# Performance work log

Hardware: AMD Instinct MI355X
Metric: run time of the kernel (lower is better)

## Reference

```python
import jax, jax.numpy as jnp
import numpy as np

B, T, D = 2, 2048, 1024
H, HD = 16, 32
INNER = H * HD
FF = 4 * D
KT, KP = 3, 15


def _layernorm(x, g, b, eps=1e-5):
    mu = jnp.mean(x, axis=-1, keepdims=True)
    var = jnp.var(x, axis=-1, keepdims=True)
    return (x - mu) * jax.lax.rsqrt(var + eps) * g + b


def _causal_dwconv(x, w, b):
    # x: (b,t,d), w: (d,1,k) depthwise kernel; causal left-pad of k-1
    k = w.shape[-1]
    xc = jnp.transpose(x, (0, 2, 1))  # (b,d,t)
    xp = jnp.pad(xc, ((0, 0), (0, 0), (k - 1, 0)))
    y = jax.lax.conv_general_dilated(
        xp, w, window_strides=(1,), padding='VALID',
        feature_group_count=x.shape[-1],
        dimension_numbers=('NCH', 'OIH', 'NCH'))
    return jnp.transpose(y + b[None, :, None], (0, 2, 1))


def _causal_linear_attention(q, k, v, mask):
    # q,k,v: (b,t,h,d); mask: (b,t)
    m = mask[:, :, None, None]
    q = (jax.nn.elu(q) + 1.0) * m
    k = (jax.nn.elu(k) + 1.0) * m
    v = v * m
    kv = jnp.einsum('bthd,bthe->bthde', k, v)
    kv_prefix = jnp.cumsum(kv, axis=1)          # (b,t,h,d,e) large intermediate
    k_prefix = jnp.cumsum(k, axis=1)
    num = jnp.einsum('bthd,bthde->bthe', q, kv_prefix)
    den = jnp.sum(q * k_prefix, axis=-1, keepdims=True)
    return (num / (den + 1e-6)) * m


def setup_inputs() -> dict:
    key = jax.random.key(0)
    ks = jax.random.split(key, 10)
    w = lambda i, shape: jax.random.normal(ks[i], shape, jnp.float32) * 0.02
    return {
        'inputs': jax.random.normal(ks[0], (B, T, D), jnp.float32),
        'mask': jnp.ones((B, T), jnp.float32),
        'ln1_g': jnp.ones((D,), jnp.float32), 'ln1_b': jnp.zeros((D,), jnp.float32),
        'W_in': w(1, (D, D + 3 * INNER)), 'b_in': jnp.zeros((D + 3 * INNER,), jnp.float32),
        'W_c': w(2, (INNER, D)), 'b_c': jnp.zeros((D,), jnp.float32),
        'w_t': w(3, (D, 1, KT)), 'b_t': jnp.zeros((D,), jnp.float32),
        'w_p': w(4, (D, 1, KP)), 'b_p': jnp.zeros((D,), jnp.float32),
        'W_mix': w(5, (3 * D, D)), 'b_mix': jnp.zeros((D,), jnp.float32),
        'ln2_g': jnp.ones((D,), jnp.float32), 'ln2_b': jnp.zeros((D,), jnp.float32),
        'W1': w(6, (D, FF)), 'b1': jnp.zeros((FF,), jnp.float32),
        'W2': w(7, (FF, D)), 'b2': jnp.zeros((D,), jnp.float32),
    }


def reference(inputs, mask, ln1_g, ln1_b, W_in, b_in, W_c, b_c, w_t, b_t,
              w_p, b_p, W_mix, b_mix, ln2_g, ln2_b, W1, b1, W2, b2):
    residual = inputs
    normed = _layernorm(inputs, ln1_g, ln1_b)
    proj = normed @ W_in + b_in
    gate, q, k, v = jnp.split(proj, [D, D + INNER, D + 2 * INNER], axis=-1)
    b, t, _ = inputs.shape
    q = q.reshape(b, t, H, HD)
    k = k.reshape(b, t, H, HD)
    v = v.reshape(b, t, H, HD)
    content = _causal_linear_attention(q, k, v, mask).reshape(b, t, INNER)
    content = content @ W_c + b_c
    temporal = _causal_dwconv(normed, w_t, b_t)
    positional = _causal_dwconv(normed, w_p, b_p)
    mixed = jnp.concatenate((content, temporal, positional), axis=-1) @ W_mix + b_mix
    mask_f = mask[:, :, None]
    out = residual + jax.nn.sigmoid(gate) * mixed  # dropout=0.0 -> identity
    out = out * mask_f
    h = _layernorm(out, ln2_g, ln2_b)
    ffn = jax.nn.gelu(h @ W1 + b1, approximate=False) @ W2 + b2
    out = out + ffn
    return out * mask_f
```

## Files before the change

kernel.cpp:

```cpp
#include <hip/hip_runtime.h>
#include <math.h>

#define BB 2
#define TT 2048
#define DD 1024
#define HH 16
#define INNERD 512
#define FFD 4096
#define NPROJ 2560
#define CATD 3072
#define MROWS (BB*TT)
#define CHUNK 64
#define NCH (TT/CHUNK)
#define BH 32

typedef __bf16 bf16;
typedef __attribute__((ext_vector_type(8))) __bf16 bf16x8;
typedef __attribute__((ext_vector_type(4))) __bf16 bf16x4;
typedef __attribute__((ext_vector_type(4))) float f32x4;

struct Part4 { void* p0; void* p1; void* p2; void* p3; };

__global__ __launch_bounds__(256) void prep_fused(
    const float* __restrict__ inputs, const float* __restrict__ ln1_g,
    const float* __restrict__ ln1_b, bf16* __restrict__ normed,
    const float* __restrict__ W_in,  bf16* __restrict__ wt_in,
    const float* __restrict__ W_c,   bf16* __restrict__ wt_c,
    const float* __restrict__ W_mix, bf16* __restrict__ wt_mix,
    const float* __restrict__ W1,    bf16* __restrict__ wt1,
    const float* __restrict__ W2,    bf16* __restrict__ wt2)
{
    int blk = blockIdx.x, tid = threadIdx.x;
    if (blk < MROWS) {
        int row = blk;
        f32x4 xv = ((const f32x4*)(inputs + (size_t)row * DD))[tid];
        float s = xv[0] + xv[1] + xv[2] + xv[3];
        float s2 = xv[0]*xv[0] + xv[1]*xv[1] + xv[2]*xv[2] + xv[3]*xv[3];
        #pragma unroll
        for (int off = 32; off > 0; off >>= 1) {
            s  += __shfl_xor(s,  off, 64);
            s2 += __shfl_xor(s2, off, 64);
        }
        __shared__ float rs[4], rs2[4];
        int wid = tid >> 6;
        if ((tid & 63) == 0) { rs[wid] = s; rs2[wid] = s2; }
        __syncthreads();
        s  = rs[0] + rs[1] + rs[2] + rs[3];
        s2 = rs2[0] + rs2[1] + rs2[2] + rs2[3];
        float mean = s * (1.0f / DD);
        float var  = s2 * (1.0f / DD) - mean * mean;
        float rstd = rsqrtf(var + 1e-5f);
        f32x4 gv = ((const f32x4*)ln1_g)[tid];
        f32x4 bv = ((const f32x4*)ln1_b)[tid];
        bf16x4 o;
        #pragma unroll
        for (int q = 0; q < 4; q++)
            o[q] = (bf16)((xv[q] - mean) * rstd * gv[q] + bv[q]);
        ((bf16x4*)(normed + (size_t)row * DD))[tid] = o;
        return;
    }
    int tb = blk - MROWS;
    const float* W; bf16* Wt; int Kd, Nd;
    if      (tb < 2560)  {             W = W_in;  Wt = wt_in;  Kd = 1024; Nd = 2560; }
    else if (tb < 3072)  { tb -= 2560; W = W_c;   Wt = wt_c;   Kd = 512;  Nd = 1024; }
    else if (tb < 6144)  { tb -= 3072; W = W_mix; Wt = wt_mix; Kd = 3072; Nd = 1024; }
    else if (tb < 10240) { tb -= 6144; W = W1;    Wt = wt1;    Kd = 1024; Nd = 4096; }
    else                 { tb -= 10240;W = W2;    Wt = wt2;    Kd = 4096; Nd = 1024; }
    int ntx = Nd >> 5;
    int nb = (tb % ntx) * 32, kb = (tb / ntx) * 32;
    __shared__ float t[32][33];
    int tx = tid & 31, ty = tid >> 5;
    #pragma unroll
    for (int r = 0; r < 32; r += 8)
        t[ty + r][tx] = W[(size_t)(kb + ty + r) * Nd + nb + tx];
    __syncthreads();
    #pragma unroll
    for (int r = 0; r < 32; r += 8)
        Wt[(size_t)(nb + ty + r) * Kd + kb + tx] = (bf16)t[tx][ty + r];
}

template<int EPI>
__global__ __launch_bounds__(256, 4) void gemm_mfma(
    const bf16* __restrict__ A,  int lda,
    const bf16* __restrict__ Bt, int ldb,
    const float* __restrict__ bias,
    bf16* __restrict__ Cb, int ldc,
    int K, Part4 part)
{
    __shared__ bf16 As[128 * 64];
    __shared__ bf16 Bs[128 * 64];
    const int tid  = threadIdx.x;
    const int wave = tid >> 6, lane = tid & 63;
    const int m0 = blockIdx.x * 128, n0 = blockIdx.y * 128;
    const int koff = blockIdx.z * K;
    A  += koff;
    Bt += koff;
    const int wr = wave >> 1, wc = wave & 1;
    const int lrow = lane >> 2;
    const int lcol = (lane & 3) * 8;
    const int fm = lane & 15;
    const int fk = (lane >> 4) * 8;

    f32x4 acc[4][4];
    #pragma unroll
    for (int i = 0; i < 4; i++)
        #pragma unroll
        for (int j = 0; j < 4; j++)
            acc[i][j] = (f32x4){0.f, 0.f, 0.f, 0.f};

    for (int k0 = 0; k0 < K; k0 += 64) {
        #pragma unroll
        for (int r = 0; r < 4; r++) {
            int c  = r * 4 + wave;
            int rc = c >> 1, kh = c & 1;
            const bf16* ga = A  + (size_t)(m0 + rc * 16 + lrow) * lda + k0 + kh * 32 + lcol;
            const bf16* gb = Bt + (size_t)(n0 + rc * 16 + lrow) * ldb + k0 + kh * 32 + lcol;
            __builtin_amdgcn_global_load_lds(
                (const __attribute__((address_space(1))) void*)ga,
                (__attribute__((address_space(3))) void*)(As + c * 512), 16, 0, 0);
            __builtin_amdgcn_global_load_lds(
                (const __attribute__((address_space(1))) void*)gb,
                (__attribute__((address_space(3))) void*)(Bs + c * 512), 16, 0, 0);
        }
        __syncthreads();
        #pragma unroll
        for (int ks = 0; ks < 2; ks++) {
            bf16x8 af[4], bfv[4];
            #pragma unroll
            for (int i = 0; i < 4; i++)
                af[i] = *(const bf16x8*)(As + (wr * 4 + i) * 1024 + ks * 512 + fm * 32 + fk);
            #pragma unroll
            for (int j = 0; j < 4; j++)
                bfv[j] = *(const bf16x8*)(Bs + (wc * 4 + j) * 1024 + ks * 512 + fm * 32 + fk);
            #pragma unroll
            for (int i = 0; i < 4; i++)
                #pragma unroll
                for (int j = 0; j < 4; j++)
                    acc[i][j] = __builtin_amdgcn_mfma_f32_16x16x32_bf16(
                        af[i], bfv[j], acc[i][j], 0, 0, 0);
        }
        __syncthreads();
    }

    void* psel = nullptr;
    if constexpr (EPI == 4) {
        int z = blockIdx.z;
        psel = (z == 0) ? part.p0 : (z == 1) ? part.p1 : (z == 2) ? part.p2 : part.p3;
    }

    #pragma unroll
    for (int i = 0; i < 4; i++) {
        int mbase = m0 + wr * 64 + i * 16 + (lane >> 4) * 4;
        #pragma unroll
        for (int j = 0; j < 4; j++) {
            int col = n0 + wc * 64 + j * 16 + (lane & 15);
            float bv = 0.f;
            if constexpr (EPI == 0 || EPI == 1) bv = bias[col];
            #pragma unroll
            for (int r = 0; r < 4; r++) {
                int row = mbase + r;
                float v = acc[i][j][r] + bv;
                if constexpr (EPI == 0) {
                    Cb[(size_t)row * ldc + col] = (bf16)v;
                } else if constexpr (EPI == 1) {
                    float z2 = v * (1.5957691f + 0.07135502f * v * v);
                    v = v / (1.0f + __expf(-z2));
                    Cb[(size_t)row * ldc + col] = (bf16)v;
                } else {
                    ((bf16*)psel)[(size_t)row * DD + col] = (bf16)v;
                }
            }
        }
    }
}

__global__ __launch_bounds__(256) void epi_wc(
    const bf16* __restrict__ P0, const bf16* __restrict__ P1,
    const float* __restrict__ bias, bf16* __restrict__ cat)
{
    int id = blockIdx.x * 256 + threadIdx.x;
    int row = id >> 8, cg = id & 255;
    bf16x4 s0 = ((const bf16x4*)P0)[id];
    bf16x4 s1 = ((const bf16x4*)P1)[id];
    f32x4 b  = ((const f32x4*)bias)[cg];
    bf16x4 o;
    #pragma unroll
    for (int q = 0; q < 4; q++) o[q] = (bf16)((float)s0[q] + (float)s1[q] + b[q]);
    *(bf16x4*)(cat + (size_t)row * CATD + cg * 4) = o;
}

__global__ __launch_bounds__(256) void epi_mix_ln2(
    const bf16* __restrict__ P0, const bf16* __restrict__ P1,
    const bf16* __restrict__ P2, const float* __restrict__ bias,
    const bf16* __restrict__ proj, const float* __restrict__ res,
    const float* __restrict__ mask,
    const float* __restrict__ g2, const float* __restrict__ b2v,
    float* __restrict__ out1, bf16* __restrict__ hbuf)
{
    int row = blockIdx.x, tid = threadIdx.x;
    float m = mask[row];
    size_t off = (size_t)row * DD + tid * 4;
    bf16x4 s0 = *(const bf16x4*)(P0 + off);
    bf16x4 s1 = *(const bf16x4*)(P1 + off);
    bf16x4 s2v = *(const bf16x4*)(P2 + off);
    f32x4 bv = ((const f32x4*)bias)[tid];
    bf16x4 g4 = *(const bf16x4*)(proj + (size_t)row * NPROJ + tid * 4);
    f32x4 rv = ((const f32x4*)(res + (size_t)row * DD))[tid];
    f32x4 v;
    #pragma unroll
    for (int q = 0; q < 4; q++) {
        float sg = 1.0f / (1.0f + __expf(-(float)g4[q]));
        float sv = (float)s0[q] + (float)s1[q] + (float)s2v[q] + bv[q];
        v[q] = (rv[q] + sg * sv) * m;
    }
    ((f32x4*)(out1 + (size_t)row * DD))[tid] = v;
    float s = v[0] + v[1] + v[2] + v[3];
    float s2 = v[0]*v[0] + v[1]*v[1] + v[2]*v[2] + v[3]*v[3];
    #pragma unroll
    for (int off2 = 32; off2 > 0; off2 >>= 1) {
        s  += __shfl_xor(s,  off2, 64);
        s2 += __shfl_xor(s2, off2, 64);
    }
    __shared__ float rs[4], rs2[4];
    int wid = tid >> 6;
    if ((tid & 63) == 0) { rs[wid] = s; rs2[wid] = s2; }
    __syncthreads();
    s  = rs[0] + rs[1] + rs[2] + rs[3];
    s2 = rs2[0] + rs2[1] + rs2[2] + rs2[3];
    float mean = s * (1.0f / DD);
    float var  = s2 * (1.0f / DD) - mean * mean;
    float rstd = rsqrtf(var + 1e-5f);
    f32x4 gg = ((const f32x4*)g2)[tid];
    f32x4 bb = ((const f32x4*)b2v)[tid];
    bf16x4 h;
    #pragma unroll
    for (int q = 0; q < 4; q++)
        h[q] = (bf16)((v[q] - mean) * rstd * gg[q] + bb[q]);
    ((bf16x4*)(hbuf + (size_t)row * DD))[tid] = h;
}

__global__ __launch_bounds__(256) void epi_w2(
    float* __restrict__ d_out, const float* __restrict__ out1,
    const bf16* __restrict__ P0, const bf16* __restrict__ P1,
    const bf16* __restrict__ P2, const bf16* __restrict__ P3,
    const float* __restrict__ bias, const float* __restrict__ mask)
{
    int id = blockIdx.x * 256 + threadIdx.x;
    int row = id >> 8;
    float m = mask[row];
    bf16x4 a0 = ((const bf16x4*)P0)[id];
    bf16x4 a1 = ((const bf16x4*)P1)[id];
    bf16x4 a2 = ((const bf16x4*)P2)[id];
    bf16x4 a3 = ((const bf16x4*)P3)[id];
    f32x4 r = ((const f32x4*)out1)[id];
    f32x4 b = ((const f32x4*)bias)[id & 255];
    f32x4 o;
    #pragma unroll
    for (int q = 0; q < 4; q++) {
        float sv = (float)a0[q] + (float)a1[q] + (float)a2[q] + (float)a3[q];
        o[q] = (r[q] + sv + b[q]) * m;
    }
    ((f32x4*)d_out)[id] = o;
}

__device__ __forceinline__ float phi_f(float x) {
    return x > 0.f ? x + 1.f : __expf(x);
}

__global__ __launch_bounds__(256) void mid_fused(
    const bf16* __restrict__ x,
    const float* __restrict__ w_t, const float* __restrict__ b_t,
    const float* __restrict__ w_p, const float* __restrict__ b_p,
    bf16* __restrict__ cat,
    const bf16* __restrict__ proj, const float* __restrict__ mask,
    float* __restrict__ kvsum, float* __restrict__ kssum)
{
    __shared__ float s_ks[2][CHUNK][32], s_vs[2][CHUNK][32];
    int blk = blockIdx.x, tid = threadIdx.x;
    if (blk < 1024) {
        int id = blk * 256 + tid;
        int cg = id & 127, rp = id >> 7;
        int c0 = cg * 8;
        int row0 = rp * 2;
        int t0 = row0 & (TT - 1);
        bf16x8 xw[16];
        #pragma unroll
        for (int j = 0; j < 16; j++) {
            int t = t0 - 14 + j;
            if (t >= 0)
                xw[j] = *(const bf16x8*)(x + (size_t)(row0 - 14 + j) * DD + c0);
            else
                #pragma unroll
                for (int q = 0; q < 8; q++) xw[j][q] = (bf16)0.f;
        }
        float y15[2][8], y3[2][8];
        #pragma unroll
        for (int q = 0; q < 8; q++) {
            float bp = b_p[c0 + q], bt = b_t[c0 + q];
            y15[0][q] = bp; y15[1][q] = bp;
            y3[0][q] = bt;  y3[1][q] = bt;
        }
        #pragma unroll
        for (int i = 0; i < 15; i++) {
            float wp[8];
            #pragma unroll
            for (int q = 0; q < 8; q++) wp[q] = w_p[(c0 + q) * 15 + i];
            #pragma unroll
            for (int rr = 0; rr < 2; rr++)
                #pragma unroll
                for (int q = 0; q < 8; q++)
                    y15[rr][q] = fmaf(wp[q], (float)xw[rr + i][q], y15[rr][q]);
        }
        #pragma unroll
        for (int i = 0; i < 3; i++) {
            float wt[8];
            #pragma unroll
            for (int q = 0; q < 8; q++) wt[q] = w_t[(c0 + q) * 3 + i];
            #pragma unroll
            for (int rr = 0; rr < 2; rr++)
                #pragma unroll
                for (int q = 0; q < 8; q++)
                    y3[rr][q] = fmaf(wt[q], (float)xw[rr + 12 + i][q], y3[rr][q]);
        }
        #pragma unroll
        for (int rr = 0; rr < 2; rr++) {
            bf16x8 o3, o15;
            #pragma unroll
            for (int q = 0; q < 8; q++) { o3[q] = (bf16)y3[rr][q]; o15[q] = (bf16)y15[rr][q]; }
            *(bf16x8*)(cat + (size_t)(row0 + rr) * CATD + DD + c0)     = o3;
            *(bf16x8*)(cat + (size_t)(row0 + rr) * CATD + 2 * DD + c0) = o15;
        }
        return;
    }
    int w = tid >> 6;
    if (w >= 2) return;
    int lane = tid & 63;
    int ci = (blk - 1024) * 2 + w;
    int c  = ci & (NCH - 1);
    int bh = ci >> 5;
    int b  = bh >> 4, hh = bh & (HH - 1);
    float (*ks)[32] = s_ks[w];
    float (*vs)[32] = s_vs[w];
    int row0 = b * TT + c * CHUNK;
    {
        int row = row0 + lane;
        float m = mask[row];
        const bf16* kp = proj + (size_t)row * NPROJ + DD + INNERD + hh * 32;
        const bf16* vp = kp + INNERD;
        #pragma unroll
        for (int s = 0; s < 4; s++) {
            bf16x8 k8 = *(const bf16x8*)(kp + s * 8);
            bf16x8 v8 = *(const bf16x8*)(vp + s * 8);
            #pragma unroll
            for (int q = 0; q < 8; q++) {
                ks[lane][s * 8 + q] = phi_f((float)k8[q]) * m;
                vs[lane][s * 8 + q] = (float)v8[q] * m;
            }
        }
    }
    int e = lane & 31, d0 = (lane >> 5) * 16;
    float kv[16], ksl[16];
    #pragma unroll
    for (int j = 0; j < 16; j++) { kv[j] = 0.f; ksl[j] = 0.f; }
    for (int t = 0; t < CHUNK; t++) {
        float ve = vs[t][e];
        f32x4 kr[4];
        #pragma unroll
        for (int s = 0; s < 4; s++) kr[s] = *(const f32x4*)&ks[t][d0 + s * 4];
        #pragma unroll
        for (int j = 0; j < 16; j++) {
            float kval = kr[j >> 2][j & 3];
            kv[j] = fmaf(kval, ve, kv[j]);
            ksl[j] += kval;
        }
    }
    size_t base = (size_t)ci * 1024;
    #pragma unroll
    for (int j = 0; j < 16; j++)
        kvsum[base + (size_t)(d0 + j) * 32 + e] = kv[j];
    if (e == 0) {
        #pragma unroll
        for (int j = 0; j < 16; j++)
            kssum[ci * 32 + d0 + j] = ksl[j];
    }
}

__global__ __launch_bounds__(256) void attn_prefix(
    const float* __restrict__ kvsum, const float* __restrict__ kssum,
    float* __restrict__ kvpref, float* __restrict__ kspref)
{
    int bh = blockIdx.x;
    int tid = threadIdx.x;
    float run[4] = {0.f, 0.f, 0.f, 0.f};
    for (int c = 0; c < NCH; c++) {
        size_t base = (size_t)(bh * NCH + c) * 1024 + tid * 4;
        #pragma unroll
        for (int q = 0; q < 4; q++) {
            kvpref[base + q] = run[q];
            run[q] += kvsum[base + q];
        }
    }
    if (tid < 32) {
        float r = 0.f;
        for (int c = 0; c < NCH; c++) {
            kspref[(bh * NCH + c) * 32 + tid] = r;
            r += kssum[(bh * NCH + c) * 32 + tid];
        }
    }
}

__global__ __launch_bounds__(64) void attn_scan(
    const bf16* __restrict__ proj, const float* __restrict__ mask,
    const float* __restrict__ kvpref, const float* __restrict__ kspref,
    bf16* __restrict__ attn_out)
{
    int blk = blockIdx.x;
    int c  = blk & (NCH - 1);
    int bh = blk >> 5;
    int b  = bh >> 4, hh = bh & (HH - 1);
    int lane = threadIdx.x;
    __shared__ float qs[CHUNK][32], ks[CHUNK][32], vs[CHUNK][32];
    __shared__ float ms[CHUNK];
    int row0 = b * TT + c * CHUNK;
    {
        int row = row0 + lane;
        float m = mask[row];
        ms[lane] = m;
        const bf16* qp = proj + (size_t)row * NPROJ + DD + hh * 32;
        const bf16* kp = qp + INNERD;
        const bf16* vp = kp + INNERD;
        #pragma unroll
        for (int s = 0; s < 4; s++) {
            bf16x8 q8 = *(const bf16x8*)(qp + s * 8);
            bf16x8 k8 = *(const bf16x8*)(kp + s * 8);
            bf16x8 v8 = *(const bf16x8*)(vp + s * 8);
            #pragma unroll
            for (int q = 0; q < 8; q++) {
                qs[lane][s * 8 + q] = phi_f((float)q8[q]) * m;
                ks[lane][s * 8 + q] = phi_f((float)k8[q]) * m;
                vs[lane][s * 8 + q] = (float)v8[q] * m;
            }
        }
    }
    int e = lane & 31, d0 = (lane >> 5) * 16;
    float kv[16], ksl[16];
    size_t base = (size_t)blk * 1024;
    #pragma unroll
    for (int j = 0; j < 16; j++) kv[j] = kvpref[base + (size_t)(d0 + j) * 32 + e];
    #pragma unroll
    for (int j = 0; j < 16; j++) ksl[j] = kspref[blk * 32 + d0 + j];
    __syncthreads();
    for (int t = 0; t < CHUNK; t++) {
        float ve = vs[t][e];
        f32x4 kr[4], qr[4];
        #pragma unroll
        for (int s = 0; s < 4; s++) kr[s] = *(const f32x4*)&ks[t][d0 + s * 4];
        #pragma unroll
        for (int s = 0; s < 4; s++) qr[s] = *(const f32x4*)&qs[t][d0 + s * 4];
        float num0 = 0.f, num1 = 0.f, den0 = 0.f, den1 = 0.f;
        #pragma unroll
        for (int j = 0; j < 16; j++) {
            float kval = kr[j >> 2][j & 3], qval = qr[j >> 2][j & 3];
            kv[j]  = fmaf(kval, ve, kv[j]);
            ksl[j] += kval;
            if (j & 1) { num1 = fmaf(qval, kv[j], num1); den1 = fmaf(qval, ksl[j], den1); }
            else       { num0 = fmaf(qval, kv[j], num0); den0 = fmaf(qval, ksl[j], den0); }
        }
        float num = num0 + num1, den = den0 + den1;
        num += __shfl_xor(num, 32, 64);
        den += __shfl_xor(den, 32, 64);
        if (lane < 32)
            attn_out[(size_t)(row0 + t) * INNERD + hh * 32 + e] =
                (bf16)(num / (den + 1e-6f) * ms[t]);
    }
}

extern "C" void kernel_launch(void* const* d_in, const int* in_sizes, int n_in,
                              void* d_out, int out_size, void* d_ws, size_t ws_size,
                              hipStream_t stream)
{
    const float* inputs = (const float*)d_in[0];
    const float* mask   = (const float*)d_in[1];
    const float* ln1_g  = (const float*)d_in[2];
    const float* ln1_b  = (const float*)d_in[3];
    const float* W_in   = (const float*)d_in[4];
    const float* b_in   = (const float*)d_in[5];
    const float* W_c    = (const float*)d_in[6];
    const float* b_c    = (const float*)d_in[7];
    const float* w_t    = (const float*)d_in[8];
    const float* b_t    = (const float*)d_in[9];
    const float* w_p    = (const float*)d_in[10];
    const float* b_p    = (const float*)d_in[11];
    const float* W_mix  = (const float*)d_in[12];
    const float* b_mix  = (const float*)d_in[13];
    const float* ln2_g  = (const float*)d_in[14];
    const float* ln2_b  = (const float*)d_in[15];
    const float* W1     = (const float*)d_in[16];
    const float* b1     = (const float*)d_in[17];
    const float* W2     = (const float*)d_in[18];
    const float* b2     = (const float*)d_in[19];
    float* out = (float*)d_out;

    char* p = (char*)d_ws;
    bf16* normed = (bf16*)p;  p += (size_t)MROWS * DD * 2;
    bf16* proj   = (bf16*)p;  p += (size_t)MROWS * NPROJ * 2;
    bf16* attnb  = (bf16*)p;  p += (size_t)MROWS * INNERD * 2;
    bf16* cat    = (bf16*)p;  p += (size_t)MROWS * CATD * 2;
    float* out1  = (float*)p; p += (size_t)MROWS * DD * 4;
    bf16* hbuf   = (bf16*)p;  p += (size_t)MROWS * DD * 2;
    bf16* wt_in  = (bf16*)p;  p += (size_t)NPROJ * DD * 2;
    bf16* wt_c   = (bf16*)p;  p += (size_t)DD * INNERD * 2;
    bf16* wt_mix = (bf16*)p;  p += (size_t)DD * CATD * 2;
    bf16* wt1    = (bf16*)p;  p += (size_t)FFD * DD * 2;
    bf16* wt2    = (bf16*)p;  p += (size_t)DD * FFD * 2;
    bf16* ffn1   = (bf16*)d_ws;
    float* kvsum = out1;
    float* kvpref= kvsum  + (size_t)BH * NCH * 1024;
    float* kssum = kvpref + (size_t)BH * NCH * 1024;
    float* kspref= kssum  + (size_t)BH * NCH * 32;
    bf16*  c_p0  = (bf16*)d_out;
    bf16*  c_p1  = (bf16*)out1;
    bf16*  m_p0  = (bf16*)d_out;
    bf16*  m_p1  = (bf16*)d_out + (size_t)MROWS * DD;
    bf16*  m_p2  = hbuf;
    bf16*  w2_p0 = cat;
    bf16*  w2_p1 = cat + (size_t)MROWS * DD;
    bf16*  w2_p2 = cat + (size_t)MROWS * DD * 2;
    bf16*  w2_p3 = hbuf;

    prep_fused<<<MROWS + 14336, 256, 0, stream>>>(
        inputs, ln1_g, ln1_b, normed,
        W_in, wt_in, W_c, wt_c, W_mix, wt_mix, W1, wt1, W2, wt2);
    gemm_mfma<0><<<dim3(MROWS/128, NPROJ/128), 256, 0, stream>>>(
        normed, DD, wt_in, DD, b_in, proj, NPROJ, DD, Part4{});
    mid_fused<<<1024 + 512, 256, 0, stream>>>(
        normed, w_t, b_t, w_p, b_p, cat, proj, mask, kvsum, kssum);
    attn_prefix<<<BH, 256, 0, stream>>>(kvsum, kssum, kvpref, kspref);
    attn_scan  <<<BH * NCH, 64, 0, stream>>>(proj, mask, kvpref, kspref, attnb);
    gemm_mfma<4><<<dim3(MROWS/128, DD/128, 2), 256, 0, stream>>>(
        attnb, INNERD, wt_c, INNERD, nullptr, nullptr, DD, INNERD / 2,
        Part4{c_p0, c_p1, nullptr, nullptr});
    epi_wc<<<MROWS * DD / 4 / 256, 256, 0, stream>>>(c_p0, c_p1, b_c, cat);
    gemm_mfma<4><<<dim3(MROWS/128, DD/128, 3), 256, 0, stream>>>(
        cat, CATD, wt_mix, CATD, nullptr, nullptr, DD, CATD / 3,
        Part4{m_p0, m_p1, m_p2, nullptr});
    epi_mix_ln2<<<MROWS, 256, 0, stream>>>(m_p0, m_p1, m_p2, b_mix, proj, inputs,
                                           mask, ln2_g, ln2_b, out1, hbuf);
    gemm_mfma<1><<<dim3(MROWS/128, FFD/128), 256, 0, stream>>>(
        hbuf, DD, wt1, DD, b1, ffn1, FFD, DD, Part4{});
    gemm_mfma<4><<<dim3(MROWS/128, DD/128, 4), 256, 0, stream>>>(
        ffn1, FFD, wt2, FFD, nullptr, nullptr, DD, FFD / 4,
        Part4{w2_p0, w2_p1, w2_p2, w2_p3});
    epi_w2<<<MROWS * DD / 4 / 256, 256, 0, stream>>>(out, out1, w2_p0, w2_p1,
                                                     w2_p2, w2_p3, b2, mask);
}
```

Baseline: 397.0 us.

## Replace GEMM with 256x256 double-buffered swizzled-LDS MFMA kernel

```diff
diff --git a/kernel.cpp b/kernel.cpp
--- a/kernel.cpp
+++ b/kernel.cpp
@@ -79,67 +79,118 @@
         Wt[(size_t)(nb + ty + r) * Kd + kb + tx] = (bf16)t[tx][ty + r];
 }
 
+__device__ __forceinline__ void stage_half(
+    const bf16* __restrict__ src, int ld, int k0, int h_row0,
+    bf16* lds_half, int wave, int rl, int ce)
+{
+    #pragma unroll
+    for (int i = 0; i < 2; i++) {
+        int R = h_row0 + (i * 8 + wave) * 8 + rl;
+        const bf16* g = src + (size_t)R * ld + k0 + ce;
+        __builtin_amdgcn_global_load_lds(
+            (const __attribute__((address_space(1))) void*)g,
+            (__attribute__((address_space(3))) void*)(lds_half + (i * 8 + wave) * 512),
+            16, 0, 0);
+    }
+}
+
+__device__ __forceinline__ bf16x8 frag_ld(const bf16* buf, int row, int col)
+{
+    int off = row * 64 + col;
+    off ^= ((row >> 2) & 1) << 4;
+    return *(const bf16x8*)(buf + off);
+}
+
 template<int EPI>
-__global__ __launch_bounds__(256, 4) void gemm_mfma(
+__global__ __launch_bounds__(512) void gemm256(
     const bf16* __restrict__ A,  int lda,
     const bf16* __restrict__ Bt, int ldb,
     const float* __restrict__ bias,
     bf16* __restrict__ Cb, int ldc,
     int K, Part4 part)
 {
-    __shared__ bf16 As[128 * 64];
-    __shared__ bf16 Bs[128 * 64];
+    __shared__ bf16 sA0[16384], sB0[16384], sA1[16384], sB1[16384];
     const int tid  = threadIdx.x;
     const int wave = tid >> 6, lane = tid & 63;
-    const int m0 = blockIdx.x * 128, n0 = blockIdx.y * 128;
-    const int koff = blockIdx.z * K;
-    A  += koff;
-    Bt += koff;
-    const int wr = wave >> 1, wc = wave & 1;
-    const int lrow = lane >> 2;
-    const int lcol = (lane & 3) * 8;
+    const int m0 = blockIdx.x * 256, n0 = blockIdx.y * 256;
+    A  += (size_t)m0 * lda + (size_t)blockIdx.z * K;
+    Bt += (size_t)n0 * ldb + (size_t)blockIdx.z * K;
+    const int wr = wave >> 2, wc = wave & 3;
+    const int rl = lane >> 3;
+    const int ce = ((lane & 7) * 8) ^ ((lane >= 32) ? 16 : 0);
     const int fm = lane & 15;
     const int fk = (lane >> 4) * 8;
 
-    f32x4 acc[4][4];
-    #pragma unroll
-    for (int i = 0; i < 4; i++)
+    f32x4 acc[8][4];
+    #pragma unroll
+    for (int i = 0; i < 8; i++)
         #pragma unroll
         for (int j = 0; j < 4; j++)
             acc[i][j] = (f32x4){0.f, 0.f, 0.f, 0.f};
 
-    for (int k0 = 0; k0 < K; k0 += 64) {
-        #pragma unroll
-        for (int r = 0; r < 4; r++) {
-            int c  = r * 4 + wave;
-            int rc = c >> 1, kh = c & 1;
-            const bf16* ga = A  + (size_t)(m0 + rc * 16 + lrow) * lda + k0 + kh * 32 + lcol;
-            const bf16* gb = Bt + (size_t)(n0 + rc * 16 + lrow) * ldb + k0 + kh * 32 + lcol;
-            __builtin_amdgcn_global_load_lds(
-                (const __attribute__((address_space(1))) void*)ga,
-                (__attribute__((address_space(3))) void*)(As + c * 512), 16, 0, 0);
-            __builtin_amdgcn_global_load_lds(
-                (const __attribute__((address_space(1))) void*)gb,
-                (__attribute__((address_space(3))) void*)(Bs + c * 512), 16, 0, 0);
-        }
-        __syncthreads();
-        #pragma unroll
-        for (int ks = 0; ks < 2; ks++) {
-            bf16x8 af[4], bfv[4];
-            #pragma unroll
-            for (int i = 0; i < 4; i++)
-                af[i] = *(const bf16x8*)(As + (wr * 4 + i) * 1024 + ks * 512 + fm * 32 + fk);
-            #pragma unroll
-            for (int j = 0; j < 4; j++)
-                bfv[j] = *(const bf16x8*)(Bs + (wc * 4 + j) * 1024 + ks * 512 + fm * 32 + fk);
-            #pragma unroll
-            for (int i = 0; i < 4; i++)
+    const int NT = K >> 6;
+    stage_half(A,  lda, 0, 0,   sA0,        wave, rl, ce);
+    stage_half(A,  lda, 0, 128, sA0 + 8192, wave, rl, ce);
+    stage_half(Bt, ldb, 0, 0,   sB0,        wave, rl, ce);
+    stage_half(Bt, ldb, 0, 128, sB0 + 8192, wave, rl, ce);
+    if (NT > 1) {
+        stage_half(A, lda, 64, 0, sA1, wave, rl, ce);
+        asm volatile("s_waitcnt vmcnt(2)" ::: "memory");
+    } else {
+        asm volatile("s_waitcnt vmcnt(0)" ::: "memory");
+    }
+    __builtin_amdgcn_s_barrier();
+
+    for (int t = 0; t < NT; t++) {
+        bf16* Ac = (t & 1) ? sA1 : sA0;
+        bf16* Bc = (t & 1) ? sB1 : sB0;
+        bf16* An = (t & 1) ? sA0 : sA1;
+        bf16* Bn = (t & 1) ? sB0 : sB1;
+        const int kn = (t + 1) << 6;
+        bf16x8 bq[4][2];
+        #pragma unroll
+        for (int p = 0; p < 4; p++) {
+            bf16x8 aq[2][2];
+            if (p == 0) {
                 #pragma unroll
                 for (int j = 0; j < 4; j++)
-                    acc[i][j] = __builtin_amdgcn_mfma_f32_16x16x32_bf16(
-                        af[i], bfv[j], acc[i][j], 0, 0, 0);
-        }
-        __syncthreads();
+                    #pragma unroll
+                    for (int ks = 0; ks < 2; ks++)
+                        bq[j][ks] = frag_ld(Bc, wc * 64 + j * 16 + fm, ks * 32 + fk);
+            }
+            #pragma unroll
+            for (int ii = 0; ii < 2; ii++)
+                #pragma unroll
+                for (int ks = 0; ks < 2; ks++)
+                    aq[ii][ks] = frag_ld(Ac, wr * 128 + (p * 2 + ii) * 16 + fm,
+                                         ks * 32 + fk);
+            if (t + 1 < NT) {
+                if (p == 0) stage_half(A,  lda, kn, 128, An + 8192, wave, rl, ce);
+                if (p == 1) stage_half(Bt, ldb, kn, 0,   Bn,        wave, rl, ce);
+                if (p == 2) stage_half(Bt, ldb, kn, 128, Bn + 8192, wave, rl, ce);
+            }
+            __builtin_amdgcn_s_barrier();
+            asm volatile("s_waitcnt lgkmcnt(0)" ::: "memory");
+            __builtin_amdgcn_sched_barrier(0);
+            __builtin_amdgcn_s_setprio(1);
+            #pragma unroll
+            for (int ii = 0; ii < 2; ii++)
+                #pragma unroll
+                for (int j = 0; j < 4; j++)
+                    #pragma unroll
+                    for (int ks = 0; ks < 2; ks++)
+                        acc[p * 2 + ii][j] = __builtin_amdgcn_mfma_f32_16x16x32_bf16(
+                            aq[ii][ks], bq[j][ks], acc[p * 2 + ii][j], 0, 0, 0);
+            __builtin_amdgcn_s_setprio(0);
+            __builtin_amdgcn_s_barrier();
+        }
+        if (t + 2 < NT)
+            stage_half(A, lda, (t + 2) << 6, 0, Ac, wave, rl, ce);
+        if (t + 1 < NT) {
+            if (t + 2 < NT) asm volatile("s_waitcnt vmcnt(2)" ::: "memory");
+            else            asm volatile("s_waitcnt vmcnt(0)" ::: "memory");
+            __builtin_amdgcn_s_barrier();
+        }
     }
 
     void* psel = nullptr;
@@ -149,11 +200,11 @@
     }
 
     #pragma unroll
-    for (int i = 0; i < 4; i++) {
-        int mbase = m0 + wr * 64 + i * 16 + (lane >> 4) * 4;
+    for (int i = 0; i < 8; i++) {
+        int mbase = m0 + wr * 128 + i * 16 + (lane >> 4) * 4;
         #pragma unroll
         for (int j = 0; j < 4; j++) {
-            int col = n0 + wc * 64 + j * 16 + (lane & 15);
+            int col = n0 + wc * 64 + j * 16 + fm;
             float bv = 0.f;
             if constexpr (EPI == 0 || EPI == 1) bv = bias[col];
             #pragma unroll
@@ -531,24 +582,24 @@
     prep_fused<<<MROWS + 14336, 256, 0, stream>>>(
         inputs, ln1_g, ln1_b, normed,
         W_in, wt_in, W_c, wt_c, W_mix, wt_mix, W1, wt1, W2, wt2);
-    gemm_mfma<0><<<dim3(MROWS/128, NPROJ/128), 256, 0, stream>>>(
+    gemm256<0><<<dim3(MROWS/256, NPROJ/256), 512, 0, stream>>>(
         normed, DD, wt_in, DD, b_in, proj, NPROJ, DD, Part4{});
     mid_fused<<<1024 + 512, 256, 0, stream>>>(
         normed, w_t, b_t, w_p, b_p, cat, proj, mask, kvsum, kssum);
     attn_prefix<<<BH, 256, 0, stream>>>(kvsum, kssum, kvpref, kspref);
     attn_scan  <<<BH * NCH, 64, 0, stream>>>(proj, mask, kvpref, kspref, attnb);
-    gemm_mfma<4><<<dim3(MROWS/128, DD/128, 2), 256, 0, stream>>>(
+    gemm256<4><<<dim3(MROWS/256, DD/256, 2), 512, 0, stream>>>(
         attnb, INNERD, wt_c, INNERD, nullptr, nullptr, DD, INNERD / 2,
         Part4{c_p0, c_p1, nullptr, nullptr});
     epi_wc<<<MROWS * DD / 4 / 256, 256, 0, stream>>>(c_p0, c_p1, b_c, cat);
-    gemm_mfma<4><<<dim3(MROWS/128, DD/128, 3), 256, 0, stream>>>(
+    gemm256<4><<<dim3(MROWS/256, DD/256, 3), 512, 0, stream>>>(
         cat, CATD, wt_mix, CATD, nullptr, nullptr, DD, CATD / 3,
         Part4{m_p0, m_p1, m_p2, nullptr});
     epi_mix_ln2<<<MROWS, 256, 0, stream>>>(m_p0, m_p1, m_p2, b_mix, proj, inputs,
                                            mask, ln2_g, ln2_b, out1, hbuf);
-    gemm_mfma<1><<<dim3(MROWS/128, FFD/128), 256, 0, stream>>>(
+    gemm256<1><<<dim3(MROWS/256, FFD/256), 512, 0, stream>>>(
         hbuf, DD, wt1, DD, b1, ffn1, FFD, DD, Part4{});
-    gemm_mfma<4><<<dim3(MROWS/128, DD/128, 4), 256, 0, stream>>>(
+    gemm256<4><<<dim3(MROWS/256, DD/256, 4), 512, 0, stream>>>(
         ffn1, FFD, wt2, FFD, nullptr, nullptr, DD, FFD / 4,
         Part4{w2_p0, w2_p1, w2_p2, w2_p3});
     epi_w2<<<MROWS * DD / 4 / 256, 256, 0, stream>>>(out, out1, w2_p0, w2_p1,
```

Result: slower. 434.2 us (+9.4%).

## Fold W_c into W_mix so attention output feeds the mix GEMM directly

Applied to the files above, without the earlier changes.

```diff
diff --git a/kernel.cpp b/kernel.cpp
--- a/kernel.cpp
+++ b/kernel.cpp
@@ -8,7 +8,7 @@
 #define INNERD 512
 #define FFD 4096
 #define NPROJ 2560
-#define CATD 3072
+#define CATD2 2560
 #define MROWS (BB*TT)
 #define CHUNK 64
 #define NCH (TT/CHUNK)
@@ -25,10 +25,11 @@
     const float* __restrict__ inputs, const float* __restrict__ ln1_g,
     const float* __restrict__ ln1_b, bf16* __restrict__ normed,
     const float* __restrict__ W_in,  bf16* __restrict__ wt_in,
-    const float* __restrict__ W_c,   bf16* __restrict__ wt_c,
-    const float* __restrict__ W_mix, bf16* __restrict__ wt_mix,
+    const float* __restrict__ W_mix, bf16* __restrict__ wt_m0,
+    bf16* __restrict__ wt_comb,
     const float* __restrict__ W1,    bf16* __restrict__ wt1,
-    const float* __restrict__ W2,    bf16* __restrict__ wt2)
+    const float* __restrict__ W2,    bf16* __restrict__ wt2,
+    const float* __restrict__ b_mix, float* __restrict__ bmix2)
 {
     int blk = blockIdx.x, tid = threadIdx.x;
     if (blk < MROWS) {
@@ -60,14 +61,22 @@
         return;
     }
     int tb = blk - MROWS;
-    const float* W; bf16* Wt; int Kd, Nd;
+    if (tb == 13824) {
+        ((f32x4*)bmix2)[tid] = ((const f32x4*)b_mix)[tid];
+        return;
+    }
+    const float* W; bf16* Wt = nullptr; int Kd, Nd; bool is_mix = false;
     if      (tb < 2560)  {             W = W_in;  Wt = wt_in;  Kd = 1024; Nd = 2560; }
-    else if (tb < 3072)  { tb -= 2560; W = W_c;   Wt = wt_c;   Kd = 512;  Nd = 1024; }
-    else if (tb < 6144)  { tb -= 3072; W = W_mix; Wt = wt_mix; Kd = 3072; Nd = 1024; }
-    else if (tb < 10240) { tb -= 6144; W = W1;    Wt = wt1;    Kd = 1024; Nd = 4096; }
-    else                 { tb -= 10240;W = W2;    Wt = wt2;    Kd = 4096; Nd = 1024; }
+    else if (tb < 5632)  { tb -= 2560; W = W_mix;              Kd = 3072; Nd = 1024; is_mix = true; }
+    else if (tb < 9728)  { tb -= 5632; W = W1;    Wt = wt1;    Kd = 1024; Nd = 4096; }
+    else                 { tb -= 9728; W = W2;    Wt = wt2;    Kd = 4096; Nd = 1024; }
     int ntx = Nd >> 5;
     int nb = (tb % ntx) * 32, kb = (tb / ntx) * 32;
+    int ldW = Kd, kw = kb;
+    if (is_mix) {
+        if (kb < 1024) { Wt = wt_m0;   ldW = 1024;  kw = kb; }
+        else           { Wt = wt_comb; ldW = CATD2; kw = kb - 512; }
+    }
     __shared__ float t[32][33];
     int tx = tid & 31, ty = tid >> 5;
     #pragma unroll
@@ -76,7 +85,32 @@
     __syncthreads();
     #pragma unroll
     for (int r = 0; r < 32; r += 8)
-        Wt[(size_t)(nb + ty + r) * Kd + kb + tx] = (bf16)t[tx][ty + r];
+        Wt[(size_t)(nb + ty + r) * ldW + kw + tx] = (bf16)t[tx][ty + r];
+}
+
+__global__ __launch_bounds__(256) void prep2(
+    const float* __restrict__ W_c, bf16* __restrict__ wc_b,
+    const float* __restrict__ b_c, const float* __restrict__ W_mix,
+    float* __restrict__ bmix2)
+{
+    int blk = blockIdx.x, tid = threadIdx.x;
+    if (blk < 512) {
+        int id = blk * 256 + tid;
+        f32x4 v = ((const f32x4*)W_c)[id];
+        bf16x4 o;
+        #pragma unroll
+        for (int q = 0; q < 4; q++) o[q] = (bf16)v[q];
+        ((bf16x4*)wc_b)[id] = o;
+        return;
+    }
+    int s = blk - 512;
+    int n  = (s & 3) * 256 + tid;
+    int j0 = (s >> 2) * 64;
+    float acc = 0.f;
+    #pragma unroll 8
+    for (int j = 0; j < 64; j++)
+        acc = fmaf(b_c[j0 + j], W_mix[(size_t)(j0 + j) * DD + n], acc);
+    atomicAdd(&bmix2[n], acc);
 }
 
 template<int EPI>
@@ -166,6 +200,8 @@
                     float z2 = v * (1.5957691f + 0.07135502f * v * v);
                     v = v / (1.0f + __expf(-z2));
                     Cb[(size_t)row * ldc + col] = (bf16)v;
+                } else if constexpr (EPI == 5) {
+                    Cb[(size_t)row * ldc + col] = (bf16)v;
                 } else {
                     ((bf16*)psel)[(size_t)row * DD + col] = (bf16)v;
                 }
@@ -174,24 +210,9 @@
     }
 }
 
-__global__ __launch_bounds__(256) void epi_wc(
-    const bf16* __restrict__ P0, const bf16* __restrict__ P1,
-    const float* __restrict__ bias, bf16* __restrict__ cat)
-{
-    int id = blockIdx.x * 256 + threadIdx.x;
-    int row = id >> 8, cg = id & 255;
-    bf16x4 s0 = ((const bf16x4*)P0)[id];
-    bf16x4 s1 = ((const bf16x4*)P1)[id];
-    f32x4 b  = ((const f32x4*)bias)[cg];
-    bf16x4 o;
-    #pragma unroll
-    for (int q = 0; q < 4; q++) o[q] = (bf16)((float)s0[q] + (float)s1[q] + b[q]);
-    *(bf16x4*)(cat + (size_t)row * CATD + cg * 4) = o;
-}
-
 __global__ __launch_bounds__(256) void epi_mix_ln2(
     const bf16* __restrict__ P0, const bf16* __restrict__ P1,
-    const bf16* __restrict__ P2, const float* __restrict__ bias,
+    const float* __restrict__ bias,
     const bf16* __restrict__ proj, const float* __restrict__ res,
     const float* __restrict__ mask,
     const float* __restrict__ g2, const float* __restrict__ b2v,
@@ -202,7 +223,6 @@
     size_t off = (size_t)row * DD + tid * 4;
     bf16x4 s0 = *(const bf16x4*)(P0 + off);
     bf16x4 s1 = *(const bf16x4*)(P1 + off);
-    bf16x4 s2v = *(const bf16x4*)(P2 + off);
     f32x4 bv = ((const f32x4*)bias)[tid];
     bf16x4 g4 = *(const bf16x4*)(proj + (size_t)row * NPROJ + tid * 4);
     f32x4 rv = ((const f32x4*)(res + (size_t)row * DD))[tid];
@@ -210,7 +230,7 @@
     #pragma unroll
     for (int q = 0; q < 4; q++) {
         float sg = 1.0f / (1.0f + __expf(-(float)g4[q]));
-        float sv = (float)s0[q] + (float)s1[q] + (float)s2v[q] + bv[q];
+        float sv = (float)s0[q] + (float)s1[q] + bv[q];
         v[q] = (rv[q] + sg * sv) * m;
     }
     ((f32x4*)(out1 + (size_t)row * DD))[tid] = v;
@@ -327,8 +347,8 @@
             bf16x8 o3, o15;
             #pragma unroll
             for (int q = 0; q < 8; q++) { o3[q] = (bf16)y3[rr][q]; o15[q] = (bf16)y15[rr][q]; }
-            *(bf16x8*)(cat + (size_t)(row0 + rr) * CATD + DD + c0)     = o3;
-            *(bf16x8*)(cat + (size_t)(row0 + rr) * CATD + 2 * DD + c0) = o15;
+            *(bf16x8*)(cat + (size_t)(row0 + rr) * CATD2 + 512 + c0)  = o3;
+            *(bf16x8*)(cat + (size_t)(row0 + rr) * CATD2 + 1536 + c0) = o15;
         }
         return;
     }
@@ -389,30 +409,32 @@
     const float* __restrict__ kvsum, const float* __restrict__ kssum,
     float* __restrict__ kvpref, float* __restrict__ kspref)
 {
-    int bh = blockIdx.x;
-    int tid = threadIdx.x;
-    float run[4] = {0.f, 0.f, 0.f, 0.f};
+    int blk = blockIdx.x, tid = threadIdx.x;
+    if (blk < 128) {
+        int bh = blk >> 2;
+        int de = (blk & 3) * 256 + tid;
+        float run = 0.f;
+        for (int c = 0; c < NCH; c++) {
+            size_t a = (size_t)(bh * NCH + c) * 1024 + de;
+            kvpref[a] = run;
+            run += kvsum[a];
+        }
+        return;
+    }
+    int id = (blk - 128) * 256 + tid;
+    int bh = id >> 5, d = id & 31;
+    float r = 0.f;
     for (int c = 0; c < NCH; c++) {
-        size_t base = (size_t)(bh * NCH + c) * 1024 + tid * 4;
-        #pragma unroll
-        for (int q = 0; q < 4; q++) {
-            kvpref[base + q] = run[q];
-            run[q] += kvsum[base + q];
-        }
-    }
-    if (tid < 32) {
-        float r = 0.f;
-        for (int c = 0; c < NCH; c++) {
-            kspref[(bh * NCH + c) * 32 + tid] = r;
-            r += kssum[(bh * NCH + c) * 32 + tid];
-        }
+        int a = (bh * NCH + c) * 32 + d;
+        kspref[a] = r;
+        r += kssum[a];
     }
 }
 
 __global__ __launch_bounds__(64) void attn_scan(
     const bf16* __restrict__ proj, const float* __restrict__ mask,
     const float* __restrict__ kvpref, const float* __restrict__ kspref,
-    bf16* __restrict__ attn_out)
+    bf16* __restrict__ cat)
 {
     int blk = blockIdx.x;
     int c  = blk & (NCH - 1);
@@ -470,7 +492,7 @@
         num += __shfl_xor(num, 32, 64);
         den += __shfl_xor(den, 32, 64);
         if (lane < 32)
-            attn_out[(size_t)(row0 + t) * INNERD + hh * 32 + e] =
+            cat[(size_t)(row0 + t) * CATD2 + hh * 32 + e] =
                 (bf16)(num / (den + 1e-6f) * ms[t]);
     }
 }
@@ -504,47 +526,44 @@
     char* p = (char*)d_ws;
     bf16* normed = (bf16*)p;  p += (size_t)MROWS * DD * 2;
     bf16* proj   = (bf16*)p;  p += (size_t)MROWS * NPROJ * 2;
-    bf16* attnb  = (bf16*)p;  p += (size_t)MROWS * INNERD * 2;
-    bf16* cat    = (bf16*)p;  p += (size_t)MROWS * CATD * 2;
+    bf16* cat    = (bf16*)p;  p += (size_t)MROWS * CATD2 * 2;
     float* out1  = (float*)p; p += (size_t)MROWS * DD * 4;
     bf16* hbuf   = (bf16*)p;  p += (size_t)MROWS * DD * 2;
     bf16* wt_in  = (bf16*)p;  p += (size_t)NPROJ * DD * 2;
-    bf16* wt_c   = (bf16*)p;  p += (size_t)DD * INNERD * 2;
-    bf16* wt_mix = (bf16*)p;  p += (size_t)DD * CATD * 2;
+    bf16* wt_m0  = (bf16*)p;  p += (size_t)DD * DD * 2;
+    bf16* wt_comb= (bf16*)p;  p += (size_t)DD * CATD2 * 2;
     bf16* wt1    = (bf16*)p;  p += (size_t)FFD * DD * 2;
     bf16* wt2    = (bf16*)p;  p += (size_t)DD * FFD * 2;
+    bf16* wc_b   = (bf16*)p;  p += (size_t)INNERD * DD * 2;
+    float* bmix2 = (float*)p; p += (size_t)DD * 4;
     bf16* ffn1   = (bf16*)d_ws;
     float* kvsum = out1;
     float* kvpref= kvsum  + (size_t)BH * NCH * 1024;
     float* kssum = kvpref + (size_t)BH * NCH * 1024;
     float* kspref= kssum  + (size_t)BH * NCH * 32;
-    bf16*  c_p0  = (bf16*)d_out;
-    bf16*  c_p1  = (bf16*)out1;
     bf16*  m_p0  = (bf16*)d_out;
     bf16*  m_p1  = (bf16*)d_out + (size_t)MROWS * DD;
-    bf16*  m_p2  = hbuf;
-    bf16*  w2_p0 = cat;
-    bf16*  w2_p1 = cat + (size_t)MROWS * DD;
-    bf16*  w2_p2 = cat + (size_t)MROWS * DD * 2;
+    bf16*  w2_p0 = (bf16*)((char*)cat + ((size_t)4  << 20));
+    bf16*  w2_p1 = (bf16*)((char*)cat + ((size_t)12 << 20));
+    bf16*  w2_p2 = wt1;
     bf16*  w2_p3 = hbuf;
 
-    prep_fused<<<MROWS + 14336, 256, 0, stream>>>(
+    prep_fused<<<MROWS + 13824 + 1, 256, 0, stream>>>(
         inputs, ln1_g, ln1_b, normed,
-        W_in, wt_in, W_c, wt_c, W_mix, wt_mix, W1, wt1, W2, wt2);
+        W_in, wt_in, W_mix, wt_m0, wt_comb, W1, wt1, W2, wt2, b_mix, bmix2);
+    prep2<<<512 + 64, 256, 0, stream>>>(W_c, wc_b, b_c, W_mix, bmix2);
     gemm_mfma<0><<<dim3(MROWS/128, NPROJ/128), 256, 0, stream>>>(
         normed, DD, wt_in, DD, b_in, proj, NPROJ, DD, Part4{});
+    gemm_mfma<5><<<dim3(DD/128, INNERD/128), 256, 0, stream>>>(
+        wt_m0, DD, wc_b, DD, nullptr, wt_comb, CATD2, DD, Part4{});
     mid_fused<<<1024 + 512, 256, 0, stream>>>(
         normed, w_t, b_t, w_p, b_p, cat, proj, mask, kvsum, kssum);
-    attn_prefix<<<BH, 256, 0, stream>>>(kvsum, kssum, kvpref, kspref);
-    attn_scan  <<<BH * NCH, 64, 0, stream>>>(proj, mask, kvpref, kspref, attnb);
+    attn_prefix<<<132, 256, 0, stream>>>(kvsum, kssum, kvpref, kspref);
+    attn_scan  <<<BH * NCH, 64, 0, stream>>>(proj, mask, kvpref, kspref, cat);
     gemm_mfma<4><<<dim3(MROWS/128, DD/128, 2), 256, 0, stream>>>(
-        attnb, INNERD, wt_c, INNERD, nullptr, nullptr, DD, INNERD / 2,
-        Part4{c_p0, c_p1, nullptr, nullptr});
-    epi_wc<<<MROWS * DD / 4 / 256, 256, 0, stream>>>(c_p0, c_p1, b_c, cat);
-    gemm_mfma<4><<<dim3(MROWS/128, DD/128, 3), 256, 0, stream>>>(
-        cat, CATD, wt_mix, CATD, nullptr, nullptr, DD, CATD / 3,
-        Part4{m_p0, m_p1, m_p2, nullptr});
-    epi_mix_ln2<<<MROWS, 256, 0, stream>>>(m_p0, m_p1, m_p2, b_mix, proj, inputs,
+        cat, CATD2, wt_comb, CATD2, nullptr, nullptr, DD, CATD2 / 2,
+        Part4{m_p0, m_p1, nullptr, nullptr});
+    epi_mix_ln2<<<MROWS, 256, 0, stream>>>(m_p0, m_p1, bmix2, proj, inputs,
                                            mask, ln2_g, ln2_b, out1, hbuf);
     gemm_mfma<1><<<dim3(MROWS/128, FFD/128), 256, 0, stream>>>(
         hbuf, DD, wt1, DD, b1, ffn1, FFD, DD, Part4{});
```

After: 410.8 us. 3.5% more time.
